# Kernel optimization log

Hardware: AMD Instinct MI355X
Metric: run time of the kernel (lower is better)

The kernel has to match this reference:

```python
import jax, jax.numpy as jnp
import numpy as np

B, L, S, H, C = 64, 512, 512, 768, 9  # batch, bert subword len, word seq len, hidden, num_classes


def setup_inputs() -> dict:
    key = jax.random.key(0)
    k1, k2, k3 = jax.random.split(key, 3)
    rng = np.random.RandomState(0)
    # per-word subword counts in {1,2,3}; truncate so totals fit in L subword slots
    lens = rng.randint(1, 4, size=(B, S))
    cum = lens.cumsum(axis=1)
    keep = cum <= L
    ids_lens = (lens * keep).astype(np.int32)
    totals = ids_lens.sum(axis=1)
    attention_mask = (np.arange(L)[None, :] < totals[:, None]).astype(np.int32)
    label_mask = ids_lens > 0
    label_ids = (rng.randint(0, C, size=(B, S)) * label_mask).astype(np.int32)
    bert_out = jax.random.normal(k1, (B, L, H), dtype=jnp.float32)
    W = jax.random.normal(k2, (H, C), dtype=jnp.float32) * 0.02
    b = jnp.zeros((C,), dtype=jnp.float32)
    return {
        "bert_out": bert_out,
        "W": W,
        "b": b,
        "attention_mask": jnp.asarray(attention_mask),
        "ids_lens": jnp.asarray(ids_lens),
        "label_ids": jnp.asarray(label_ids),
        "label_mask": jnp.asarray(label_mask),
    }


def reference(bert_out, W, b, attention_mask, ids_lens, label_ids, label_mask):
    Bv, Lv, Hv = bert_out.shape
    Sv = ids_lens.shape[1]
    nseg = Bv * Sv
    am = attention_mask.astype(jnp.int32)
    # subword position within each example's valid region
    sidx = jnp.cumsum(am, axis=1) - 1                       # [B, L]
    # word index for each subword: searchsorted into cumulative word lengths
    ends = jnp.cumsum(ids_lens, axis=1)                     # [B, S]
    widx = jax.vmap(lambda e, s: jnp.searchsorted(e, s, side='right'))(ends, sidx)
    seg = jnp.where(am > 0, widx + jnp.arange(Bv)[:, None] * Sv, nseg)  # pad bucket = nseg
    flat = bert_out.reshape(Bv * Lv, Hv)
    segf = seg.reshape(Bv * Lv)
    sums = jax.ops.segment_sum(flat, segf, num_segments=nseg + 1)[:nseg]
    cnts = jax.ops.segment_sum(jnp.ones((Bv * Lv,), bert_out.dtype), segf,
                               num_segments=nseg + 1)[:nseg]
    mean = sums / jnp.maximum(cnts, 1.0)[:, None]           # segment mean (split().mean(0))
    word_mask = (ids_lens > 0).reshape(nseg)
    embed = jnp.where(word_mask[:, None], mean, 0.0).reshape(Bv, Sv, Hv)  # masked_scatter
    # dropout in eval mode = identity
    logits = embed @ W + b                                  # [B, S, C]
    logp = jax.nn.log_softmax(logits, axis=-1)
    lab = jnp.clip(label_ids, 0, W.shape[1] - 1)
    nll = -jnp.take_along_axis(logp, lab[..., None].astype(jnp.int32), axis=-1)[..., 0]
    valid = label_mask.astype(bert_out.dtype)
    loss = jnp.sum(nll * valid) / jnp.maximum(jnp.sum(valid), 1.0)
    pred = jnp.argmax(logits, axis=-1)
    return loss, pred
```

## Files before the change

### kernel.cpp

```cpp
#include <hip/hip_runtime.h>

#define BB 64
#define LL 512
#define SS 512
#define HH 768
#define CC 9
#define NROWS (BB * LL)
#define NWORDS (BB * SS)
#define RLS 12
#define WTPAD 772
#define R1_BLOCKS 1024
#define ROWS_PER_BLOCK 32

template <int CTRL>
__device__ __forceinline__ float dpp_add(float x) {
    int y = __builtin_amdgcn_update_dpp(0, __float_as_int(x), CTRL, 0xf, 0xf, true);
    return x + __int_as_float(y);
}
__device__ __forceinline__ float rsum64(float x) {
    x = dpp_add<0x111>(x);
    x = dpp_add<0x112>(x);
    x = dpp_add<0x114>(x);
    x = dpp_add<0x118>(x);
    x = dpp_add<0x142>(x);
    x = dpp_add<0x143>(x);
    return x;
}

__global__ __launch_bounds__(256) void row_gemm_kernel(
    const float* __restrict__ bert,
    const float* __restrict__ Wm,
    float* __restrict__ RL,
    float* __restrict__ accum)
{
    __shared__ __align__(16) float WT[CC][WTPAD];

    for (int i = threadIdx.x; i < HH * CC; i += 256) {
        int h = i / CC;
        int c = i - h * CC;
        WT[c][h] = Wm[i];
    }
    __syncthreads();

    int wave = threadIdx.x >> 6;
    int lane = threadIdx.x & 63;
    int hoff = lane * 4;

    float4 wreg[CC][3];
#pragma unroll
    for (int c = 0; c < CC; c++)
#pragma unroll
        for (int c3 = 0; c3 < 3; c3++)
            wreg[c][c3] = *reinterpret_cast<const float4*>(&WT[c][c3 * 256 + hoff]);

    size_t row0 = (size_t)blockIdx.x * ROWS_PER_BLOCK + wave * 8;

#pragma unroll
    for (int r = 0; r < 8; ++r) {
        const float* p = bert + (row0 + r) * HH + hoff;
        float4 f0 = *reinterpret_cast<const float4*>(p);
        float4 f1 = *reinterpret_cast<const float4*>(p + 256);
        float4 f2 = *reinterpret_cast<const float4*>(p + 512);

        float acc[CC];
#pragma unroll
        for (int c = 0; c < CC; c++) {
            acc[c] = f0.x * wreg[c][0].x + f0.y * wreg[c][0].y
                   + f0.z * wreg[c][0].z + f0.w * wreg[c][0].w
                   + f1.x * wreg[c][1].x + f1.y * wreg[c][1].y
                   + f1.z * wreg[c][1].z + f1.w * wreg[c][1].w
                   + f2.x * wreg[c][2].x + f2.y * wreg[c][2].y
                   + f2.z * wreg[c][2].z + f2.w * wreg[c][2].w;
        }
#pragma unroll
        for (int c = 0; c < CC; c++) acc[c] = rsum64(acc[c]);

        if (lane == 63) {
            float* dst = RL + (row0 + r) * RLS;
            float4 s0; s0.x = acc[0]; s0.y = acc[1]; s0.z = acc[2]; s0.w = acc[3];
            float4 s1; s1.x = acc[4]; s1.y = acc[5]; s1.z = acc[6]; s1.w = acc[7];
            *reinterpret_cast<float4*>(dst) = s0;
            *reinterpret_cast<float4*>(dst + 4) = s1;
            dst[8] = acc[8];
        }
    }

    if (blockIdx.x == 0 && threadIdx.x == 0) {
        accum[0] = 0.0f;
        accum[1] = 0.0f;
        ((int*)accum)[2] = 0;
    }
}

__global__ __launch_bounds__(512) void pool_kernel(
    const float* __restrict__ RL,
    const float* __restrict__ bias,
    const int* __restrict__ ids_lens,
    const int* __restrict__ label_ids,
    float* __restrict__ pred_out,
    float* __restrict__ accum,
    float* __restrict__ out_loss)
{
    __shared__ int sbuf[SS];
    __shared__ float swn[8], swc[8];

    int b = blockIdx.x, t = threadIdx.x;
    int lane = t & 63, wave = t >> 6;

    int v = ids_lens[b * SS + t];
    sbuf[t] = v;
    __syncthreads();
    for (int off = 1; off < SS; off <<= 1) {
        int x = (t >= off) ? sbuf[t - off] : 0;
        __syncthreads();
        sbuf[t] += x;
        __syncthreads();
    }
    int len = v;
    int start = sbuf[t] - v;

    float s[CC];
#pragma unroll
    for (int c = 0; c < CC; c++) s[c] = 0.0f;

    const float* rl = RL + ((size_t)b * LL + start) * RLS;
    for (int j = 0; j < len; ++j) {
        const float* p = rl + j * RLS;
        float4 a = *reinterpret_cast<const float4*>(p);
        float4 c4 = *reinterpret_cast<const float4*>(p + 4);
        float e = p[8];
        s[0] += a.x;  s[1] += a.y;  s[2] += a.z;  s[3] += a.w;
        s[4] += c4.x; s[5] += c4.y; s[6] += c4.z; s[7] += c4.w;
        s[8] += e;
    }

    float inv = 1.0f / (float)(len > 0 ? len : 1);
    float lg[CC];
#pragma unroll
    for (int c = 0; c < CC; c++) lg[c] = s[c] * inv + bias[c];

    float mx = lg[0];
    int arg = 0;
#pragma unroll
    for (int c = 1; c < CC; c++) {
        if (lg[c] > mx) { mx = lg[c]; arg = c; }
    }
    float se = 0.0f;
#pragma unroll
    for (int c = 0; c < CC; c++) se += expf(lg[c] - mx);
    float lse = mx + logf(se);

    int lab = label_ids[b * SS + t];
    lab = lab < 0 ? 0 : (lab > CC - 1 ? CC - 1 : lab);
    float valid = (len > 0) ? 1.0f : 0.0f;
    float nll = (lse - lg[lab]) * valid;

    pred_out[b * SS + t] = (float)arg;

    float rn = rsum64(nll);
    float rc = rsum64(valid);
    if (lane == 63) { swn[wave] = rn; swc[wave] = rc; }
    __syncthreads();
    if (t == 0) {
        float bn = 0.0f, bc = 0.0f;
#pragma unroll
        for (int i = 0; i < 8; i++) { bn += swn[i]; bc += swc[i]; }
        atomicAdd(accum, bn);
        atomicAdd(accum + 1, bc);
        __threadfence();
        int old = atomicAdd((int*)accum + 2, 1);
        if (old == BB - 1) {
            float tn = atomicAdd(accum, 0.0f);
            float tc = atomicAdd(accum + 1, 0.0f);
            out_loss[0] = tn / fmaxf(tc, 1.0f);
        }
    }
}

extern "C" void kernel_launch(void* const* d_in, const int* in_sizes, int n_in,
                              void* d_out, int out_size, void* d_ws, size_t ws_size,
                              hipStream_t stream) {
    const float* bert = (const float*)d_in[0];
    const float* Wm   = (const float*)d_in[1];
    const float* bias = (const float*)d_in[2];
    const int* ids_lens  = (const int*)d_in[4];
    const int* label_ids = (const int*)d_in[5];

    float* out = (float*)d_out;

    float* RL    = (float*)d_ws;
    float* accum = RL + (size_t)NROWS * RLS;

    row_gemm_kernel<<<R1_BLOCKS, 256, 0, stream>>>(bert, Wm, RL, accum);
    pool_kernel<<<BB, SS, 0, stream>>>(RL, bias, ids_lens, label_ids,
                                       out + 1, accum, out);
}
```

Baseline: 170.5 us.

## Fuse row projection with word pooling and skip padded subword rows

Merges the per-row projection and the per-word pooling into one kernel where each block handles 32 words, computes its starting subword offset from ids_lens, and projects only the rows belonging to those words into shared memory. Padding rows beyond the attention region are no longer read, roughly halving the memory traffic on bert_out, and the global round trip for row logits disappears. A small finalize kernel sums per-block partials instead of using atomics. The dynamic row loop loses the fixed unrolling and adds a redundant prefix scan per block.

```diff
diff --git a/kernel.cpp b/kernel.cpp
--- a/kernel.cpp
+++ b/kernel.cpp
@@ -5,12 +5,11 @@
 #define SS 512
 #define HH 768
 #define CC 9
-#define NROWS (BB * LL)
-#define NWORDS (BB * SS)
-#define RLS 12
+#define WPB 32
+#define NBLK (BB * SS / WPB)
+#define MAXROWS (WPB * 3)
 #define WTPAD 772
-#define R1_BLOCKS 1024
-#define ROWS_PER_BLOCK 32
+#define RLST 12
 
 template <int CTRL>
 __device__ __forceinline__ float dpp_add(float x) {
@@ -27,25 +26,54 @@
     return x;
 }
 
-__global__ __launch_bounds__(256) void row_gemm_kernel(
+__global__ __launch_bounds__(256) void fused_kernel(
     const float* __restrict__ bert,
     const float* __restrict__ Wm,
-    float* __restrict__ RL,
-    float* __restrict__ accum)
+    const float* __restrict__ bias,
+    const int* __restrict__ ids_lens,
+    const int* __restrict__ label_ids,
+    float* __restrict__ pred_out,
+    float* __restrict__ nll_part,
+    float* __restrict__ cnt_part)
 {
     __shared__ __align__(16) float WT[CC][WTPAD];
-
-    for (int i = threadIdx.x; i < HH * CC; i += 256) {
+    __shared__ __align__(16) float RLs[MAXROWS][RLST];
+    __shared__ int wlen[WPB], woff[WPB];
+    __shared__ int s_meta[2];
+    __shared__ float red[4];
+
+    int b = blockIdx.x >> 4;
+    int q = blockIdx.x & 15;
+    int w0 = q * WPB;
+    const int* lens = ids_lens + b * SS;
+
+    int t = threadIdx.x, lane = t & 63, wave = t >> 6;
+
+    for (int i = t; i < HH * CC; i += 256) {
         int h = i / CC;
         int c = i - h * CC;
         WT[c][h] = Wm[i];
     }
-    __syncthreads();
-
-    int wave = threadIdx.x >> 6;
-    int lane = threadIdx.x & 63;
+    if (t < WPB) wlen[t] = lens[w0 + t];
+
+    int part = 0;
+    for (int i = t; i < w0; i += 256) part += lens[i];
+    float pf = rsum64((float)part);
+    if (lane == 63) red[wave] = pf;
+    __syncthreads();
+    if (t == 0) {
+        int start0 = (int)(red[0] + red[1] + red[2] + red[3]);
+        int run = 0;
+#pragma unroll
+        for (int k = 0; k < WPB; k++) { woff[k] = run; run += wlen[k]; }
+        s_meta[0] = start0;
+        s_meta[1] = run;
+    }
+    __syncthreads();
+    int start0 = s_meta[0];
+    int rows_n = s_meta[1];
+
     int hoff = lane * 4;
-
     float4 wreg[CC][3];
 #pragma unroll
     for (int c = 0; c < CC; c++)
@@ -53,11 +81,8 @@
         for (int c3 = 0; c3 < 3; c3++)
             wreg[c][c3] = *reinterpret_cast<const float4*>(&WT[c][c3 * 256 + hoff]);
 
-    size_t row0 = (size_t)blockIdx.x * ROWS_PER_BLOCK + wave * 8;
-
-#pragma unroll
-    for (int r = 0; r < 8; ++r) {
-        const float* p = bert + (row0 + r) * HH + hoff;
+    for (int r = wave; r < rows_n; r += 4) {
+        const float* p = bert + ((size_t)(b * LL + start0 + r)) * HH + hoff;
         float4 f0 = *reinterpret_cast<const float4*>(p);
         float4 f1 = *reinterpret_cast<const float4*>(p + 256);
         float4 f2 = *reinterpret_cast<const float4*>(p + 512);
@@ -76,104 +101,82 @@
         for (int c = 0; c < CC; c++) acc[c] = rsum64(acc[c]);
 
         if (lane == 63) {
-            float* dst = RL + (row0 + r) * RLS;
             float4 s0; s0.x = acc[0]; s0.y = acc[1]; s0.z = acc[2]; s0.w = acc[3];
             float4 s1; s1.x = acc[4]; s1.y = acc[5]; s1.z = acc[6]; s1.w = acc[7];
-            *reinterpret_cast<float4*>(dst) = s0;
-            *reinterpret_cast<float4*>(dst + 4) = s1;
-            dst[8] = acc[8];
-        }
-    }
-
-    if (blockIdx.x == 0 && threadIdx.x == 0) {
-        accum[0] = 0.0f;
-        accum[1] = 0.0f;
-        ((int*)accum)[2] = 0;
-    }
-}
-
-__global__ __launch_bounds__(512) void pool_kernel(
-    const float* __restrict__ RL,
-    const float* __restrict__ bias,
-    const int* __restrict__ ids_lens,
-    const int* __restrict__ label_ids,
-    float* __restrict__ pred_out,
-    float* __restrict__ accum,
-    float* __restrict__ out_loss)
-{
-    __shared__ int sbuf[SS];
-    __shared__ float swn[8], swc[8];
-
-    int b = blockIdx.x, t = threadIdx.x;
-    int lane = t & 63, wave = t >> 6;
-
-    int v = ids_lens[b * SS + t];
-    sbuf[t] = v;
-    __syncthreads();
-    for (int off = 1; off < SS; off <<= 1) {
-        int x = (t >= off) ? sbuf[t - off] : 0;
-        __syncthreads();
-        sbuf[t] += x;
-        __syncthreads();
-    }
-    int len = v;
-    int start = sbuf[t] - v;
-
-    float s[CC];
-#pragma unroll
-    for (int c = 0; c < CC; c++) s[c] = 0.0f;
-
-    const float* rl = RL + ((size_t)b * LL + start) * RLS;
-    for (int j = 0; j < len; ++j) {
-        const float* p = rl + j * RLS;
-        float4 a = *reinterpret_cast<const float4*>(p);
-        float4 c4 = *reinterpret_cast<const float4*>(p + 4);
-        float e = p[8];
-        s[0] += a.x;  s[1] += a.y;  s[2] += a.z;  s[3] += a.w;
-        s[4] += c4.x; s[5] += c4.y; s[6] += c4.z; s[7] += c4.w;
-        s[8] += e;
-    }
-
-    float inv = 1.0f / (float)(len > 0 ? len : 1);
-    float lg[CC];
-#pragma unroll
-    for (int c = 0; c < CC; c++) lg[c] = s[c] * inv + bias[c];
-
-    float mx = lg[0];
-    int arg = 0;
-#pragma unroll
-    for (int c = 1; c < CC; c++) {
-        if (lg[c] > mx) { mx = lg[c]; arg = c; }
-    }
-    float se = 0.0f;
-#pragma unroll
-    for (int c = 0; c < CC; c++) se += expf(lg[c] - mx);
-    float lse = mx + logf(se);
-
-    int lab = label_ids[b * SS + t];
-    lab = lab < 0 ? 0 : (lab > CC - 1 ? CC - 1 : lab);
-    float valid = (len > 0) ? 1.0f : 0.0f;
-    float nll = (lse - lg[lab]) * valid;
-
-    pred_out[b * SS + t] = (float)arg;
-
-    float rn = rsum64(nll);
-    float rc = rsum64(valid);
-    if (lane == 63) { swn[wave] = rn; swc[wave] = rc; }
+            *reinterpret_cast<float4*>(&RLs[r][0]) = s0;
+            *reinterpret_cast<float4*>(&RLs[r][4]) = s1;
+            RLs[r][8] = acc[8];
+        }
+    }
+    __syncthreads();
+
+    if (t < 64) {
+        int k = t;
+        bool active = k < WPB;
+        int len = active ? wlen[k] : 0;
+        int off = active ? woff[k] : 0;
+
+        float s[CC];
+#pragma unroll
+        for (int c = 0; c < CC; c++) s[c] = 0.0f;
+        for (int j = 0; j < len; ++j) {
+            const float* p = &RLs[off + j][0];
+            float4 a = *reinterpret_cast<const float4*>(p);
+            float4 c4 = *reinterpret_cast<const float4*>(p + 4);
+            s[0] += a.x;  s[1] += a.y;  s[2] += a.z;  s[3] += a.w;
+            s[4] += c4.x; s[5] += c4.y; s[6] += c4.z; s[7] += c4.w;
+            s[8] += p[8];
+        }
+        float inv = 1.0f / (float)(len > 0 ? len : 1);
+        float lg[CC];
+#pragma unroll
+        for (int c = 0; c < CC; c++) lg[c] = s[c] * inv + bias[c];
+
+        float mx = lg[0];
+        int arg = 0;
+#pragma unroll
+        for (int c = 1; c < CC; c++) {
+            if (lg[c] > mx) { mx = lg[c]; arg = c; }
+        }
+        float se = 0.0f;
+#pragma unroll
+        for (int c = 0; c < CC; c++) se += expf(lg[c] - mx);
+        float lse = mx + logf(se);
+
+        int g = b * SS + w0 + (active ? k : 0);
+        int lab = label_ids[g];
+        lab = lab < 0 ? 0 : (lab > CC - 1 ? CC - 1 : lab);
+        float valid = (active && len > 0) ? 1.0f : 0.0f;
+        float nll = (lse - lg[lab]) * valid;
+
+        if (active) pred_out[g] = (float)arg;
+
+        float rn = rsum64(nll);
+        float rc = rsum64(valid);
+        if (t == 63) {
+            nll_part[blockIdx.x] = rn;
+            cnt_part[blockIdx.x] = rc;
+        }
+    }
+}
+
+__global__ __launch_bounds__(1024) void finalize_kernel(
+    const float* __restrict__ nll_part,
+    const float* __restrict__ cnt_part,
+    float* __restrict__ out_loss) {
+    __shared__ float sn[16], sc[16];
+    int t = threadIdx.x, lane = t & 63, wave = t >> 6;
+    float n = nll_part[t];
+    float c = cnt_part[t];
+    n = rsum64(n);
+    c = rsum64(c);
+    if (lane == 63) { sn[wave] = n; sc[wave] = c; }
     __syncthreads();
     if (t == 0) {
-        float bn = 0.0f, bc = 0.0f;
-#pragma unroll
-        for (int i = 0; i < 8; i++) { bn += swn[i]; bc += swc[i]; }
-        atomicAdd(accum, bn);
-        atomicAdd(accum + 1, bc);
-        __threadfence();
-        int old = atomicAdd((int*)accum + 2, 1);
-        if (old == BB - 1) {
-            float tn = atomicAdd(accum, 0.0f);
-            float tc = atomicAdd(accum + 1, 0.0f);
-            out_loss[0] = tn / fmaxf(tc, 1.0f);
-        }
+        float tn = 0.0f, tc = 0.0f;
+#pragma unroll
+        for (int i = 0; i < 16; i++) { tn += sn[i]; tc += sc[i]; }
+        out_loss[0] = tn / fmaxf(tc, 1.0f);
     }
 }
 
@@ -188,10 +191,10 @@
 
     float* out = (float*)d_out;
 
-    float* RL    = (float*)d_ws;
-    float* accum = RL + (size_t)NROWS * RLS;
-
-    row_gemm_kernel<<<R1_BLOCKS, 256, 0, stream>>>(bert, Wm, RL, accum);
-    pool_kernel<<<BB, SS, 0, stream>>>(RL, bias, ids_lens, label_ids,
-                                       out + 1, accum, out);
-}
+    float* nll_part = (float*)d_ws;
+    float* cnt_part = nll_part + NBLK;
+
+    fused_kernel<<<NBLK, 256, 0, stream>>>(bert, Wm, bias, ids_lens, label_ids,
+                                           out + 1, nll_part, cnt_part);
+    finalize_kernel<<<1, 1024, 0, stream>>>(nll_part, cnt_part, out);
+}
```

Result: slower. 177.6 us (+4.1%).
